# Kernel optimization log

Measured on AMD Instinct MI355X. Metric: run time of the kernel, lower is better.

The kernel has to match this reference:

```python
import jax, jax.numpy as jnp
import numpy as np

N_PROT = 100_000; E_PROT = 1_600_000
N_LIG = 5_000;    E_LIG = 80_000
B_PROT = 64; B_LIG = 1
SEQ = 130; D = 45; K = 4; DIN = 74
PROT_DIMS = [DIN, 50, 45, 45]
LIG_DIMS  = [DIN, 50, 45, 45, 45]
HEAD = [SEQ * D, 2000, 1000, 500, 1]


def setup_inputs() -> dict:
    key = jax.random.key(0)
    ks = iter(jax.random.split(key, 64))
    def rn(shape, scale=1.0):
        return jax.random.normal(next(ks), shape, jnp.float32) * scale
    inp = {
        "prot_x": rn((N_PROT, DIN)),
        "lig_x": rn((N_LIG, DIN)),
    }
    for pref, dims in (("prot", PROT_DIMS), ("lig", LIG_DIMS)):
        for i in range(len(dims) - 1):
            fan_in = (K + 1) * dims[i]
            inp[f"{pref}_W{i}"] = rn((fan_in, dims[i + 1]), fan_in ** -0.5)
            inp[f"{pref}_b{i}"] = jnp.zeros((dims[i + 1],), jnp.float32)
    inp["qkv_w"] = rn((D, 3 * D), D ** -0.5)
    inp["qkv_b"] = jnp.zeros((3 * D,), jnp.float32)
    inp["proj_w"] = rn((D, D), D ** -0.5)
    inp["proj_b"] = jnp.zeros((D,), jnp.float32)
    for i in range(3):
        inp[f"h{i}_w"] = rn((HEAD[i], HEAD[i + 1]), HEAD[i] ** -0.5)
        inp[f"h{i}_b"] = jnp.zeros((HEAD[i + 1],), jnp.float32)
    inp["fc_w"] = rn((HEAD[3], HEAD[4]), HEAD[3] ** -0.5)
    inp["fc_b"] = jnp.zeros((HEAD[4],), jnp.float32)
    inp["prot_src"] = jax.random.randint(next(ks), (E_PROT,), 0, N_PROT, jnp.int32)
    inp["prot_dst"] = jax.random.randint(next(ks), (E_PROT,), 0, N_PROT, jnp.int32)
    # deterministic contiguous subgraph ids guarantee all 64 pockets are non-empty
    inp["prot_gid"] = (jnp.arange(N_PROT) * B_PROT // N_PROT).astype(jnp.int32)
    inp["lig_src"] = jax.random.randint(next(ks), (E_LIG,), 0, N_LIG, jnp.int32)
    inp["lig_dst"] = jax.random.randint(next(ks), (E_LIG,), 0, N_LIG, jnp.int32)
    inp["lig_gid"] = jnp.zeros((N_LIG,), jnp.int32)
    inp["training"] = 0
    return inp


def _tagconv(x, src, dst, W, b, n):
    # DGL TAGConv: h_{k+1} = D^{-1/2} A D^{-1/2} h_k ; out = [h_0..h_K] @ W + b
    deg = jax.ops.segment_sum(jnp.ones_like(dst, x.dtype), dst, num_segments=n)
    norm = jnp.where(deg > 0, deg, 1.0) ** -0.5  # clamp(min=1)^-0.5
    hops = [x]
    h = x
    for _ in range(K):
        h = norm[:, None] * jax.ops.segment_sum((h * norm[:, None])[src], dst, num_segments=n)
        hops.append(h)
    return jnp.concatenate(hops, axis=-1) @ W + b


def _l2norm(x):
    # F.normalize(dim=1): x / max(||x||_2, eps)
    return x / jnp.maximum(jnp.linalg.norm(x, axis=1, keepdims=True), 1e-12)


def _gnn(x, src, dst, gid, Ws, bs, n, ngraphs):
    for W, b in zip(Ws, bs):
        x = _l2norm(jax.nn.relu(_tagconv(x, src, dst, W, b, n)))
        # dropout is identity in eval mode
    return jax.ops.segment_max(x, gid, num_segments=ngraphs)  # DGL MaxPooling


def reference(prot_x, lig_x,
              prot_W0, prot_b0, prot_W1, prot_b1, prot_W2, prot_b2,
              lig_W0, lig_b0, lig_W1, lig_b1, lig_W2, lig_b2, lig_W3, lig_b3,
              qkv_w, qkv_b, proj_w, proj_b,
              h0_w, h0_b, h1_w, h1_b, h2_w, h2_b, fc_w, fc_b,
              prot_src, prot_dst, prot_gid, lig_src, lig_dst, lig_gid, training):
    prot_rep = _gnn(prot_x, prot_src, prot_dst, prot_gid,
                    [prot_W0, prot_W1, prot_W2], [prot_b0, prot_b1, prot_b2],
                    N_PROT, B_PROT)                    # [B_PROT, 45]
    lig_rep = _gnn(lig_x, lig_src, lig_dst, lig_gid,
                   [lig_W0, lig_W1, lig_W2, lig_W3], [lig_b0, lig_b1, lig_b2, lig_b3],
                   N_LIG, B_LIG)                       # [B_LIG, 45]
    n_seq = B_LIG + B_PROT
    seq = jnp.concatenate([lig_rep, prot_rep], axis=0)  # [n_seq, 45]
    seq = jnp.pad(seq, ((0, SEQ - n_seq), (0, 0)))[None]  # [1, 130, 45]

    # eye-based mask exactly as the torch code builds it
    idx = jnp.arange(SEQ)
    valid = idx < n_seq
    mask = jnp.eye(SEQ, dtype=jnp.float32) * (valid[:, None] & valid[None, :])
    mask = mask.at[:, n_seq - 1].set(1.0)
    mask = mask.at[n_seq - 1, :].set(1.0)
    mask = mask.at[n_seq - 1, n_seq - 1].set(0.0)

    qkv = seq @ qkv_w + qkv_b                 # [1, 130, 135]
    q, k, v = jnp.split(qkv, 3, axis=-1)      # single head, head_dim = 45
    attn = jnp.einsum("bqd,bkd->bqk", q, k) * (D ** -0.5)
    attn = jnp.where(mask[None] == 0, -1e9, attn)
    attn = jax.nn.softmax(attn, axis=-1)
    out = jnp.einsum("bqk,bkd->bqd", attn, v) @ proj_w + proj_b  # [1,130,45]

    out = out.reshape(1, SEQ * D)             # [1, 5850]
    for w, b in ((h0_w, h0_b), (h1_w, h1_b), (h2_w, h2_b)):
        out = jax.nn.relu(out @ w + b)        # head dropout off in eval
    return jax.nn.sigmoid(out @ fc_w + fc_b)  # [1, 1]
```

## Files before the change

kernel.cpp:

```cpp
#include <hip/hip_runtime.h>
#include <hip/hip_fp16.h>
#include <cstddef>
#include <cstdint>

namespace {

constexpr int NPROT = 100000;
constexpr int EPROT = 1600000;
constexpr int NLIG  = 5000;
constexpr int ELIG  = 80000;


__global__ void hist_kernel(const int* __restrict__ dst, int* __restrict__ cnt, int e) {
  int i = blockIdx.x * 256 + threadIdx.x;
  if (i < e) atomicAdd(&cnt[dst[i]], 1);
}

__global__ void scan1_kernel(const int* __restrict__ cnt, int* __restrict__ rp,
                             int* __restrict__ bsum, float* __restrict__ nrm, int n) {
  __shared__ int wsum[4];
  int t = threadIdx.x;
  int base = blockIdx.x * 1024 + t * 4;
  int v0 = 0, v1 = 0, v2 = 0, v3 = 0;
  if (base + 3 < n) {
    int4 val = *(const int4*)(cnt + base);
    v0 = val.x; v1 = val.y; v2 = val.z; v3 = val.w;
  } else if (base < n) {
    v0 = cnt[base];
    if (base + 1 < n) v1 = cnt[base + 1];
    if (base + 2 < n) v2 = cnt[base + 2];
  }
  if (base < n)     nrm[base]     = 1.0f / sqrtf(fmaxf((float)v0, 1.0f));
  if (base + 1 < n) nrm[base + 1] = 1.0f / sqrtf(fmaxf((float)v1, 1.0f));
  if (base + 2 < n) nrm[base + 2] = 1.0f / sqrtf(fmaxf((float)v2, 1.0f));
  if (base + 3 < n) nrm[base + 3] = 1.0f / sqrtf(fmaxf((float)v3, 1.0f));
  int ts = v0 + v1 + v2 + v3;
  int lane = t & 63, wv = t >> 6;
  int incl = ts;
  #pragma unroll
  for (int off = 1; off < 64; off <<= 1) {
    int o = __shfl_up(incl, off, 64);
    if (lane >= off) incl += o;
  }
  if (lane == 63) wsum[wv] = incl;
  __syncthreads();
  int woff = 0;
  #pragma unroll
  for (int i = 0; i < 4; ++i) if (i < wv) woff += wsum[i];
  int excl = woff + incl - ts;
  int o0 = excl, o1 = o0 + v0, o2 = o1 + v1, o3 = o2 + v2;
  if (base + 3 < n) {
    *(int4*)(rp + base) = make_int4(o0, o1, o2, o3);
  } else if (base < n) {
    rp[base] = o0;
    if (base + 1 < n) rp[base + 1] = o1;
    if (base + 2 < n) rp[base + 2] = o2;
  }
  if (t == 255) bsum[blockIdx.x] = woff + incl;
}

__global__ void scan2_kernel(int* __restrict__ bsum, int nb, int* __restrict__ rp_end) {
  __shared__ int s[256];
  int t = threadIdx.x;
  int v = (t < nb) ? bsum[t] : 0;
  s[t] = v;
  __syncthreads();
  int val = v;
  for (int off = 1; off < 256; off <<= 1) {
    int add = (t >= off) ? s[t - off] : 0;
    __syncthreads();
    val += add;
    s[t] = val;
    __syncthreads();
  }
  if (t < nb) bsum[t] = val - v;
  if (t == 255) *rp_end = val;
}

__global__ void scan3_kernel(int* __restrict__ rp, const int* __restrict__ bsum, int n) {
  int i = blockIdx.x * 256 + threadIdx.x;
  if (i < n) rp[i] += bsum[i >> 10];
}

__global__ void scatter_kernel(const int* __restrict__ src, const int* __restrict__ dst,
                               const int* __restrict__ rp, int* __restrict__ cur,
                               int* __restrict__ col, int e) {
  int i = blockIdx.x * 256 + threadIdx.x;
  if (i < e) {
    int d = dst[i];
    int p = rp[d] + atomicAdd(&cur[d], 1);
    col[p] = src[i];
  }
}


__device__ __forceinline__ float2 cvt_h2(uint32_t u) {
  __half2 h = *reinterpret_cast<__half2*>(&u);
  return make_float2(__low2float(h), __high2float(h));
}

__global__ void gather_all_kernel(const __half* __restrict__ gin, const int* __restrict__ rp,
                                  const int* __restrict__ col, const float* __restrict__ nrm,
                                  __half* __restrict__ gout, int n, int nbn) {
  int pass = blockIdx.x / nbn;
  int bid = blockIdx.x - pass * nbn;
  int lane = threadIdx.x & 63, wv = threadIdx.x >> 6;
  int q = lane >> 4, r = lane & 15;
  int e_slot = r >> 2, f4 = r & 3;
  int v = bid * 16 + wv * 4 + q;
  bool vok = (v < n);
  int beg = 0, deg = 0;
  if (vok) { beg = rp[v]; deg = rp[v + 1] - beg; }
  const __half* gc = gin + (size_t)pass * n * 16;
  __half* go = gout + (size_t)pass * n * 16;
  float a0 = 0.f, a1 = 0.f, a2 = 0.f, a3 = 0.f;
  for (int base = 0; __any(base < deg); base += 16) {
    int ec = (base + r < deg) ? col[beg + base + r] : -1;
    #pragma unroll
    for (int js = 0; js < 16; js += 4) {
      int sl = (q << 4) + js + e_slot;
      int s0 = __shfl(ec, sl, 64);
      int idx = (s0 >= 0) ? s0 : 0;
      float m = (s0 >= 0) ? 1.f : 0.f;
      uint2 u = *(const uint2*)(gc + (size_t)idx * 16 + (f4 << 2));
      float2 p0 = cvt_h2(u.x), p1 = cvt_h2(u.y);
      a0 += m * p0.x; a1 += m * p0.y; a2 += m * p1.x; a3 += m * p1.y;
    }
  }
  a0 += __shfl_xor(a0, 4, 64);  a1 += __shfl_xor(a1, 4, 64);
  a2 += __shfl_xor(a2, 4, 64);  a3 += __shfl_xor(a3, 4, 64);
  a0 += __shfl_xor(a0, 8, 64);  a1 += __shfl_xor(a1, 8, 64);
  a2 += __shfl_xor(a2, 8, 64);  a3 += __shfl_xor(a3, 8, 64);
  if (vok && e_slot == 0) {
    float nm = nrm[v];
    float nm2 = nm * nm;
    __half2 w0 = __floats2half2_rn(a0 * nm2, a1 * nm2);
    __half2 w1 = __floats2half2_rn(a2 * nm2, a3 * nm2);
    uint2 st;
    st.x = *reinterpret_cast<uint32_t*>(&w0);
    st.y = *reinterpret_cast<uint32_t*>(&w1);
    *(uint2*)(go + ((size_t)v << 4) + (f4 << 2)) = st;
  }
}

template<int DIN>
__global__ void init_g0_kernel(const float* __restrict__ x, const float* __restrict__ nrm,
                               __half* __restrict__ g0, int n) {
  constexpr int PD = (DIN + 15) & ~15;
  int lane = threadIdx.x & 63;
  int v = blockIdx.x * 4 + (threadIdx.x >> 6);
  if (v >= n) return;
  float nm = nrm[v];
  for (int f = lane; f < PD; f += 64) {
    float val = (f < DIN) ? x[(size_t)v * DIN + f] * nm : 0.f;
    g0[(((size_t)(f >> 4) * n + v) << 4) + (f & 15)] = __float2half(val);
  }
}

__global__ void padw_kernel(const float* __restrict__ W, float* __restrict__ Wp,
                            int din, int dout, int pd) {
  int i = blockIdx.x * 256 + threadIdx.x;
  int total = 5 * pd * dout;
  if (i >= total) return;
  int f = i / dout, j = i - f * dout;
  int hop = f / pd, rem = f - hop * pd;
  Wp[i] = (rem < din) ? W[(size_t)(hop * din + rem) * dout + j] : 0.f;
}

template<int DIN, int DOUT, bool LAST>
__global__ __launch_bounds__(256) void combine_kernel(
    const __half* __restrict__ gbase, const float* __restrict__ nrm,
    const float* __restrict__ Wp, const float* __restrict__ bias,
    __half* __restrict__ gnext, float* __restrict__ Xout, int n) {
  constexpr int PD  = (DIN + 15) & ~15;
  constexpr int NCH = PD / 16;
  constexpr int PDN = (DOUT + 15) & ~15;
  constexpr int QO  = ((DOUT + 7) / 8) * 2;
  __shared__ float ssq[4 * 64];
  int lane = threadIdx.x & 63, wv = threadIdx.x >> 6;
  int v = blockIdx.x * 64 + lane;
  bool vok = (v < n);
  int vc = vok ? v : 0;
  const size_t slabh = (size_t)n * 80;
  int cofs = __builtin_amdgcn_readfirstlane(wv) * QO;
  float acc[QO];
  #pragma unroll
  for (int jj = 0; jj < QO; ++jj) acc[jj] = 0.f;
  const float* wb = Wp + cofs;
  for (int hop = 0; hop < 5; ++hop) {
    const __half* hrow = gbase + (size_t)hop * slabh + ((size_t)vc << 4);
    #pragma unroll 1
    for (int ch = 0; ch < NCH; ++ch) {
      uint4 u0 = *(const uint4*)hrow;
      uint4 u1 = *(const uint4*)(hrow + 8);
      float h[16];
      {
        float2 p;
        p = cvt_h2(u0.x); h[0] = p.x; h[1] = p.y;
        p = cvt_h2(u0.y); h[2] = p.x; h[3] = p.y;
        p = cvt_h2(u0.z); h[4] = p.x; h[5] = p.y;
        p = cvt_h2(u0.w); h[6] = p.x; h[7] = p.y;
        p = cvt_h2(u1.x); h[8] = p.x; h[9] = p.y;
        p = cvt_h2(u1.y); h[10] = p.x; h[11] = p.y;
        p = cvt_h2(u1.z); h[12] = p.x; h[13] = p.y;
        p = cvt_h2(u1.w); h[14] = p.x; h[15] = p.y;
      }
      #pragma unroll
      for (int s = 0; s < 16; ++s) {
        #pragma unroll
        for (int jj = 0; jj < QO; ++jj) acc[jj] += h[s] * wb[s * DOUT + jj];
      }
      wb += 16 * DOUT;
      hrow += ((size_t)n << 4);
    }
  }
  float rn = 1.f / nrm[vc];
  float ss = 0.f;
  #pragma unroll
  for (int jj = 0; jj < QO; ++jj) {
    int j = cofs + jj;
    float y = (j < DOUT) ? fmaxf(bias[j] + acc[jj] * rn, 0.f) : 0.f;
    acc[jj] = y;
    ss += y * y;
  }
  ssq[wv * 64 + lane] = ss;
  __syncthreads();
  if (!vok) return;
  float tot = ssq[lane] + ssq[64 + lane] + ssq[128 + lane] + ssq[192 + lane];
  float sc = 1.f / fmaxf(sqrtf(tot), 1e-12f);
  if (LAST) {
    #pragma unroll
    for (int jj = 0; jj < QO; ++jj) {
      int j = cofs + jj;
      if (j < DOUT) Xout[(size_t)v * DOUT + j] = acc[jj] * sc;
    }
  } else {
    float nm = nrm[v];
    #pragma unroll
    for (int jj = 0; jj < QO; jj += 2) {
      int j0 = cofs + jj;
      float a = (j0 < DOUT) ? acc[jj] * sc * nm : 0.f;
      float b = (j0 + 1 < DOUT) ? acc[jj + 1] * sc * nm : 0.f;
      int ch = j0 >> 4, s = j0 & 15;
      *(__half2*)(gnext + (((size_t)ch * n + v) << 4) + s) = __floats2half2_rn(a, b);
    }
    if (wv == 3) {
      #pragma unroll
      for (int j0 = 4 * QO; j0 < PDN; j0 += 2) {
        int ch = j0 >> 4, s = j0 & 15;
        *(__half2*)(gnext + (((size_t)ch * n + v) << 4) + s) = __floats2half2_rn(0.f, 0.f);
      }
    }
  }
}


template<int DIN, int GS, int DOUT>
__global__ void init_gemm_kernel(const float* __restrict__ x, const float* __restrict__ nrm,
                                 const float* __restrict__ W, const float* __restrict__ bias,
                                 __half* __restrict__ gout, float* __restrict__ y, int n) {
  int lane = threadIdx.x & 63;
  int v = blockIdx.x * 4 + (threadIdx.x >> 6);
  if (v >= n) return;
  float nm = nrm[v];
  const float* xr = x + (size_t)v * DIN;
  float hA = (lane < DIN) ? xr[lane] : 0.f;
  float hB = 0.f;
  if constexpr (DIN > 64) { if (lane + 64 < DIN) hB = xr[lane + 64]; }
  __half* go = gout + (size_t)v * GS;
  if (lane < DIN) go[lane] = __float2half(hA * nm);
  if constexpr (DIN > 64) { if (lane + 64 < DIN) go[lane + 64] = __float2half(hB * nm); }
  int cl = (lane < DOUT) ? lane : 0;
  float acc = bias[cl];
  const float* Wk = W + cl;
  #pragma unroll
  for (int f = 0; f < DIN; ++f) {
    float hf = (f < 64) ? __shfl(hA, f, 64) : __shfl(hB, f - 64, 64);
    acc += hf * Wk[(size_t)f * DOUT];
  }
  if (lane < DOUT) y[(size_t)v * DOUT + lane] = acc;
}

template<int DIN, int GS, int DOUT, bool WRITEG, bool FINAL>
__global__ void fused_hop_kernel(const __half* __restrict__ gin, const int* __restrict__ rp,
                                 const int* __restrict__ col, const float* __restrict__ nrm,
                                 const float* __restrict__ W, __half* __restrict__ gout,
                                 float* __restrict__ y, float* __restrict__ Xout,
                                 int k, int n) {
  int lane = threadIdx.x & 63;
  int v = blockIdx.x * 4 + (threadIdx.x >> 6);
  if (v >= n) return;
  int beg = rp[v], end = rp[v + 1];
  float a0 = 0.f, a1 = 0.f;
  for (int base = beg; base < end; base += 64) {
    int m = end - base; if (m > 64) m = 64;
    int myc = (lane < m) ? col[base + lane] : 0;
    int j = 0;
    for (; j + 8 <= m; j += 8) {
      int ss[8];
      float t0[8], t1[8];
      #pragma unroll
      for (int u = 0; u < 8; ++u) ss[u] = __shfl(myc, j + u, 64);
      #pragma unroll
      for (int u = 0; u < 8; ++u) {
        const __half* rr = gin + (size_t)ss[u] * GS;
        t0[u] = (lane < DIN) ? __half2float(rr[lane]) : 0.f;
        if constexpr (DIN > 64) t1[u] = (lane + 64 < DIN) ? __half2float(rr[lane + 64]) : 0.f;
      }
      #pragma unroll
      for (int u = 0; u < 8; ++u) {
        a0 += t0[u];
        if constexpr (DIN > 64) a1 += t1[u];
      }
    }
    for (; j < m; ++j) {
      int s = __shfl(myc, j, 64);
      const __half* rr = gin + (size_t)s * GS;
      if (lane < DIN) a0 += __half2float(rr[lane]);
      if constexpr (DIN > 64) { if (lane + 64 < DIN) a1 += __half2float(rr[lane + 64]); }
    }
  }
  float nm = nrm[v];
  float hA = a0 * nm, hB = a1 * nm;
  if (WRITEG) {
    __half* go = gout + (size_t)v * GS;
    if (lane < DIN) go[lane] = __float2half(hA * nm);
    if constexpr (DIN > 64) { if (lane + 64 < DIN) go[lane + 64] = __float2half(hB * nm); }
  }
  int cl = (lane < DOUT) ? lane : 0;
  float acc = 0.f;
  if (lane < DOUT) acc = y[(size_t)v * DOUT + lane];
  const float* Wk = W + (size_t)k * DIN * DOUT + cl;
  #pragma unroll
  for (int f = 0; f < DIN; ++f) {
    float hf = (f < 64) ? __shfl(hA, f, 64) : __shfl(hB, f - 64, 64);
    acc += hf * Wk[(size_t)f * DOUT];
  }
  if constexpr (FINAL) {
    float val = (lane < DOUT) ? fmaxf(acc, 0.f) : 0.f;
    float ss2 = val * val;
    #pragma unroll
    for (int off2 = 32; off2 > 0; off2 >>= 1) ss2 += __shfl_xor(ss2, off2, 64);
    float scale = 1.f / fmaxf(sqrtf(ss2), 1e-12f);
    if (lane < DOUT) Xout[(size_t)v * DOUT + lane] = val * scale;
  } else {
    if (lane < DOUT) y[(size_t)v * DOUT + lane] = acc;
  }
}

__global__ void segmax_kernel(const float* __restrict__ X, const int* __restrict__ gid,
                              float* __restrict__ rep, int n, int row_off) {
  __shared__ float tab[4][45];
  __shared__ int gids[256];
  int t = threadIdx.x;
  for (int i = t; i < 4 * 45; i += 256) ((float*)tab)[i] = 0.f;
  int v0 = blockIdx.x * 256;
  int vend = v0 + 256; if (vend > n) vend = n;
  int nv = vend - v0;
  if (t < nv) gids[t] = gid[v0 + t];
  __syncthreads();
  int g0 = gids[0];
  int total = nv * 45;
  for (int i = t; i < total; i += 256) {
    int vl = i / 45, j = i - vl * 45;
    float val = X[(size_t)(v0 + vl) * 45 + j];
    int rel = gids[vl] - g0;
    if (rel >= 0 && rel < 4)
      atomicMax((unsigned int*)&tab[rel][j], __float_as_uint(val));
    else
      atomicMax((unsigned int*)&rep[(size_t)(row_off + gids[vl]) * 45 + j], __float_as_uint(val));
  }
  __syncthreads();
  for (int i = t; i < 4 * 45; i += 256) {
    float val = ((float*)tab)[i];
    if (val > 0.f) {
      int rel = i / 45, j = i - rel * 45;
      atomicMax((unsigned int*)&rep[(size_t)(row_off + g0 + rel) * 45 + j], __float_as_uint(val));
    }
  }
}


__global__ void qkv_kernel(const float* __restrict__ rep, const float* __restrict__ w,
                           const float* __restrict__ b, float* __restrict__ qkv) {
  int i = blockIdx.x;
  int t = threadIdx.x;
  __shared__ float sr[45];
  if (t < 45) sr[t] = (i < 65) ? rep[(size_t)i * 45 + t] : 0.f;
  __syncthreads();
  if (t < 135) {
    float acc = b[t];
    #pragma unroll 5
    for (int d = 0; d < 45; ++d) acc += sr[d] * w[d * 135 + t];
    qkv[(size_t)i * 135 + t] = acc;
  }
}

__global__ void attn_kernel(const float* __restrict__ qkv, const float* __restrict__ proj_w,
                            const float* __restrict__ proj_b, float* __restrict__ ctx) {
  int i = blockIdx.x;
  int t = threadIdx.x;
  __shared__ float q[45];
  __shared__ float p[130];
  __shared__ float red[256];
  __shared__ float ao[45];
  if (t < 45) q[t] = qkv[(size_t)i * 135 + t];
  __syncthreads();
  float s = -1e30f;
  if (t < 130) {
    int j = t;
    float dot = 0.f;
    #pragma unroll 5
    for (int d = 0; d < 45; ++d) dot += q[d] * qkv[(size_t)j * 135 + 45 + d];
    dot *= 0.14907119849998599f;
    bool mz;
    if (i == 64 && j == 64) mz = true;
    else if (i == 64 || j == 64) mz = false;
    else mz = !(i == j && i < 65);
    s = mz ? -1e9f : dot;
  }
  red[t] = s;
  __syncthreads();
  #pragma unroll
  for (int off = 128; off > 0; off >>= 1) {
    if (t < off) red[t] = fmaxf(red[t], red[t + off]);
    __syncthreads();
  }
  float mx = red[0];
  __syncthreads();
  float e = (t < 130) ? expf(s - mx) : 0.f;
  red[t] = e;
  __syncthreads();
  #pragma unroll
  for (int off = 128; off > 0; off >>= 1) {
    if (t < off) red[t] += red[t + off];
    __syncthreads();
  }
  float denom = red[0];
  __syncthreads();
  if (t < 130) p[t] = e / denom;
  __syncthreads();
  if (t < 45) {
    float acc = 0.f;
    for (int j = 0; j < 130; ++j) acc += p[j] * qkv[(size_t)j * 135 + 90 + t];
    ao[t] = acc;
  }
  __syncthreads();
  if (t < 45) {
    float pr = proj_b[t];
    #pragma unroll 5
    for (int e2 = 0; e2 < 45; ++e2) pr += ao[e2] * proj_w[e2 * 45 + t];
    ctx[(size_t)i * 45 + t] = pr;
  }
}


__global__ void bias_init_kernel(const float* __restrict__ b, float* __restrict__ out, int n) {
  int i = blockIdx.x * 256 + threadIdx.x;
  if (i < n) out[i] = b[i];
}

template<bool RELU_IN>
__global__ void fc_splitk_kernel(const float* __restrict__ x, const float* __restrict__ W,
                                 float* __restrict__ out, int nin, int nout, int kchunk) {
  __shared__ float xs[1024];
  int k0 = blockIdx.y * kchunk;
  int k1 = k0 + kchunk; if (k1 > nin) k1 = nin;
  int len = k1 - k0;
  for (int i = threadIdx.x; i < len; i += blockDim.x) {
    float v = x[k0 + i];
    xs[i] = RELU_IN ? fmaxf(v, 0.f) : v;
  }
  __syncthreads();
  int j = blockIdx.x * blockDim.x + threadIdx.x;
  if (j < nout) {
    float acc = 0.f;
    const float* Wp = W + (size_t)k0 * nout + j;
    for (int i = 0; i < len; ++i) acc += xs[i] * Wp[(size_t)i * nout];
    atomicAdd(&out[j], acc);
  }
}

__global__ void final_fc_kernel(const float* __restrict__ x, const float* __restrict__ W,
                                const float* __restrict__ b, float* __restrict__ out) {
  __shared__ float red[512];
  int t = threadIdx.x;
  float acc = 0.f;
  if (t < 500) acc = fmaxf(x[t], 0.f) * W[t];
  red[t] = acc;
  __syncthreads();
  #pragma unroll
  for (int off = 256; off > 0; off >>= 1) {
    if (t < off) red[t] += red[t + off];
    __syncthreads();
  }
  if (t == 0) {
    float z = red[0] + b[0];
    out[0] = 1.f / (1.f + expf(-z));
  }
}


struct Bufs {
  __half* slabs;
  __half *ligA, *ligB;
  float *X, *Y, *nrm, *Wp;
  int *cnt, *cur, *rp, *col, *bsum;
};

template<int DIN, int DOUT, bool LAST>
void run_layer_prot(const Bufs& g, const float* W, const float* b, int n, hipStream_t st) {
  constexpr int PD = (DIN + 15) & ~15;
  constexpr int NPASS = PD / 16;
  int nbn = (n + 15) / 16;
  size_t slabh = (size_t)n * 80;
  for (int k = 1; k <= 4; ++k)
    gather_all_kernel<<<NPASS * nbn, 256, 0, st>>>(g.slabs + (size_t)(k - 1) * slabh,
                                                   g.rp, g.col, g.nrm,
                                                   g.slabs + (size_t)k * slabh, n, nbn);
  int wtotal = 5 * PD * DOUT;
  padw_kernel<<<(wtotal + 255) / 256, 256, 0, st>>>(W, g.Wp, DIN, DOUT, PD);
  combine_kernel<DIN, DOUT, LAST><<<(n + 63) / 64, 256, 0, st>>>(
      g.slabs, g.nrm, g.Wp, b, g.slabs, g.X, n);
}

template<int DIN, int GS, int DOUT>
void run_layer_lig(const float* xin, const Bufs& g, const float* W, const float* b,
                   int n, hipStream_t st) {
  int nb = (n + 3) / 4;
  init_gemm_kernel<DIN, GS, DOUT><<<nb, 256, 0, st>>>(xin, g.nrm, W, b, g.ligA, g.Y, n);
  const __half* gin = g.ligA;
  __half* gout = g.ligB;
  for (int k = 1; k <= 4; ++k) {
    if (k < 4)
      fused_hop_kernel<DIN, GS, DOUT, true, false><<<nb, 256, 0, st>>>(gin, g.rp, g.col, g.nrm, W, gout, g.Y, g.X, k, n);
    else
      fused_hop_kernel<DIN, GS, DOUT, false, true><<<nb, 256, 0, st>>>(gin, g.rp, g.col, g.nrm, W, gout, g.Y, g.X, 4, n);
    __half* t = (__half*)gin; gin = gout; gout = t;
  }
}

void build_csr(const int* src, const int* dst, const Bufs& g, int n, int e, hipStream_t st) {
  hipMemsetAsync(g.cnt, 0, (size_t)n * 4, st);
  hipMemsetAsync(g.cur, 0, (size_t)n * 4, st);
  hist_kernel<<<(e + 255) / 256, 256, 0, st>>>(dst, g.cnt, e);
  int nb1 = (n + 1023) / 1024;
  scan1_kernel<<<nb1, 256, 0, st>>>(g.cnt, g.rp, g.bsum, g.nrm, n);
  scan2_kernel<<<1, 256, 0, st>>>(g.bsum, nb1, g.rp + n);
  scan3_kernel<<<(n + 255) / 256, 256, 0, st>>>(g.rp, g.bsum, n);
  scatter_kernel<<<(e + 255) / 256, 256, 0, st>>>(src, dst, g.rp, g.cur, g.col, e);
}

}

extern "C" void kernel_launch(void* const* d_in, const int* in_sizes, int n_in,
                              void* d_out, int out_size, void* d_ws, size_t ws_size,
                              hipStream_t stream) {
  (void)in_sizes; (void)n_in; (void)out_size;

  const float* prot_x = (const float*)d_in[0];
  const float* lig_x  = (const float*)d_in[1];
  const float* pW[3] = {(const float*)d_in[2], (const float*)d_in[4], (const float*)d_in[6]};
  const float* pB[3] = {(const float*)d_in[3], (const float*)d_in[5], (const float*)d_in[7]};
  const float* lW[4] = {(const float*)d_in[8], (const float*)d_in[10], (const float*)d_in[12], (const float*)d_in[14]};
  const float* lB[4] = {(const float*)d_in[9], (const float*)d_in[11], (const float*)d_in[13], (const float*)d_in[15]};
  const float* qkv_w = (const float*)d_in[16];
  const float* qkv_b = (const float*)d_in[17];
  const float* proj_w = (const float*)d_in[18];
  const float* proj_b = (const float*)d_in[19];
  const float* h0_w = (const float*)d_in[20];
  const float* h0_b = (const float*)d_in[21];
  const float* h1_w = (const float*)d_in[22];
  const float* h1_b = (const float*)d_in[23];
  const float* h2_w = (const float*)d_in[24];
  const float* h2_b = (const float*)d_in[25];
  const float* fc_w = (const float*)d_in[26];
  const float* fc_b = (const float*)d_in[27];
  const int* prot_src = (const int*)d_in[28];
  const int* prot_dst = (const int*)d_in[29];
  const int* prot_gid = (const int*)d_in[30];
  const int* lig_src  = (const int*)d_in[31];
  const int* lig_dst  = (const int*)d_in[32];
  const int* lig_gid  = (const int*)d_in[33];

  char* w = (char*)d_ws;
  size_t off = 0;
  auto alloc = [&](size_t bytes) -> void* {
    void* p = w + off;
    off += (bytes + 255) & ~(size_t)255;
    return p;
  };
  __half* slabs = (__half*)alloc((size_t)5 * NPROT * 80 * 2);
  __half* ligA  = (__half*)alloc((size_t)NLIG * 96 * 2);
  __half* ligB  = (__half*)alloc((size_t)NLIG * 96 * 2);
  float* X   = (float*)alloc((size_t)NPROT * 45 * 4);
  float* Y   = (float*)alloc((size_t)NLIG * 50 * 4);
  float* nrm = (float*)alloc((size_t)NPROT * 4);
  float* Wp  = (float*)alloc((size_t)5 * 80 * 50 * 4 + 256);
  int* cnt   = (int*)alloc((size_t)NPROT * 4);
  int* cur   = (int*)alloc((size_t)NPROT * 4);
  int* rp    = (int*)alloc(((size_t)NPROT + 1) * 4);
  int* colb  = (int*)alloc((size_t)EPROT * 4);
  int* bsum  = (int*)alloc((size_t)256 * 4);
  float* rep = (float*)alloc((size_t)65 * 45 * 4);
  float* qkvb = (float*)alloc((size_t)130 * 135 * 4);
  float* ctx  = (float*)alloc((size_t)5850 * 4);
  float* hb0  = (float*)alloc((size_t)2000 * 4);
  float* hb1  = (float*)alloc((size_t)1000 * 4);
  float* hb2  = (float*)alloc((size_t)500 * 4);
  if (off > ws_size) return;

  hipMemsetAsync(rep, 0, (size_t)65 * 45 * 4, stream);

  Bufs g{slabs, ligA, ligB, X, Y, nrm, Wp, cnt, cur, rp, colb, bsum};

  build_csr(prot_src, prot_dst, g, NPROT, EPROT, stream);
  init_g0_kernel<74><<<(NPROT + 3) / 4, 256, 0, stream>>>(prot_x, g.nrm, g.slabs, NPROT);
  run_layer_prot<74, 50, false>(g, pW[0], pB[0], NPROT, stream);
  run_layer_prot<50, 45, false>(g, pW[1], pB[1], NPROT, stream);
  run_layer_prot<45, 45, true >(g, pW[2], pB[2], NPROT, stream);
  segmax_kernel<<<(NPROT + 255) / 256, 256, 0, stream>>>(g.X, prot_gid, rep, NPROT, 1);

  build_csr(lig_src, lig_dst, g, NLIG, ELIG, stream);
  run_layer_lig<74, 96, 50>(lig_x, g, lW[0], lB[0], NLIG, stream);
  run_layer_lig<50, 64, 45>(g.X, g, lW[1], lB[1], NLIG, stream);
  run_layer_lig<45, 64, 45>(g.X, g, lW[2], lB[2], NLIG, stream);
  run_layer_lig<45, 64, 45>(g.X, g, lW[3], lB[3], NLIG, stream);
  segmax_kernel<<<(NLIG + 255) / 256, 256, 0, stream>>>(g.X, lig_gid, rep, NLIG, 0);

  qkv_kernel<<<130, 256, 0, stream>>>(rep, qkv_w, qkv_b, qkvb);
  attn_kernel<<<130, 256, 0, stream>>>(qkvb, proj_w, proj_b, ctx);

  bias_init_kernel<<<8, 256, 0, stream>>>(h0_b, hb0, 2000);
  fc_splitk_kernel<false><<<dim3(8, 8), 256, 0, stream>>>(ctx, h0_w, hb0, 5850, 2000, 732);
  bias_init_kernel<<<4, 256, 0, stream>>>(h1_b, hb1, 1000);
  fc_splitk_kernel<true><<<dim3(4, 4), 256, 0, stream>>>(hb0, h1_w, hb1, 2000, 1000, 500);
  bias_init_kernel<<<2, 256, 0, stream>>>(h2_b, hb2, 500);
  fc_splitk_kernel<true><<<dim3(2, 2), 256, 0, stream>>>(hb1, h2_w, hb2, 1000, 500, 500);
  final_fc_kernel<<<1, 512, 0, stream>>>(hb2, fc_w, fc_b, (float*)d_out);
}
```

Before: 1.422 ms.

## Degree-sort vertices for gather and bucket edges before CSR scatter

Builds a permutation of vertices sorted by in-degree using a counting sort, and the gather kernel now processes vertices in that order so 4-vertex groups within a wavefront have similar degree and less divergence. Edge scatter becomes two passes: edges are first binned by destination range into a temporary buffer reusing the slab memory, then scattered into CSR, so the col writes are more local. The gather inner loop also exits early once all lanes pass their degree and uses fmaf. This adds several small kernels and an extra pass over the edges, and the vertex permutation makes gather output writes scattered.

```diff
diff --git a/kernel.cpp b/kernel.cpp
--- a/kernel.cpp
+++ b/kernel.cpp
@@ -82,14 +82,80 @@
   if (i < n) rp[i] += bsum[i >> 10];
 }
 
-__global__ void scatter_kernel(const int* __restrict__ src, const int* __restrict__ dst,
-                               const int* __restrict__ rp, int* __restrict__ cur,
-                               int* __restrict__ col, int e) {
+
+__global__ void dhist_kernel(const int* __restrict__ cnt, int* __restrict__ dh, int n) {
+  int i = blockIdx.x * 256 + threadIdx.x;
+  if (i < n) atomicAdd(&dh[min(cnt[i], 255)], 1);
+}
+
+__global__ void dscan_kernel(const int* __restrict__ dh, int* __restrict__ dcur) {
+  __shared__ int s[256];
+  int t = threadIdx.x;
+  int v = dh[t];
+  s[t] = v;
+  __syncthreads();
+  int val = v;
+  for (int off = 1; off < 256; off <<= 1) {
+    int add = (t >= off) ? s[t - off] : 0;
+    __syncthreads();
+    val += add;
+    s[t] = val;
+    __syncthreads();
+  }
+  dcur[t] = val - v;
+}
+
+__global__ void dscat_kernel(const int* __restrict__ cnt, int* __restrict__ dcur,
+                             int* __restrict__ vorder, int n) {
+  int i = blockIdx.x * 256 + threadIdx.x;
+  if (i < n) {
+    int b = min(cnt[i], 255);
+    int p = atomicAdd(&dcur[b], 1);
+    vorder[p] = i;
+  }
+}
+
+
+__global__ void gcur_init_kernel(const int* __restrict__ rp, int* __restrict__ gcur, int n) {
+  int t = threadIdx.x;
+  if (t < 64) gcur[t] = rp[min(t << 11, n)];
+}
+
+__global__ void scat1_kernel(const int* __restrict__ src, const int* __restrict__ dst,
+                             int* __restrict__ gcur, uint2* __restrict__ ebuf, int e) {
+  __shared__ int lh[64], lb[64];
+  int t = threadIdx.x;
+  if (t < 64) lh[t] = 0;
+  __syncthreads();
+  int base = blockIdx.x * 4096;
+  int d[16], rk[16];
+  #pragma unroll
+  for (int j = 0; j < 16; ++j) {
+    int i = base + j * 256 + t;
+    if (i < e) {
+      d[j] = dst[i];
+      rk[j] = atomicAdd(&lh[min(d[j] >> 11, 63)], 1);
+    }
+  }
+  __syncthreads();
+  if (t < 64 && lh[t] > 0) lb[t] = atomicAdd(&gcur[t], lh[t]);
+  __syncthreads();
+  #pragma unroll
+  for (int j = 0; j < 16; ++j) {
+    int i = base + j * 256 + t;
+    if (i < e)
+      ebuf[lb[min(d[j] >> 11, 63)] + rk[j]] = make_uint2((unsigned)src[i], (unsigned)d[j]);
+  }
+}
+
+__global__ void scat2_kernel(const uint2* __restrict__ ebuf, const int* __restrict__ rp,
+                             int* __restrict__ cur, int* __restrict__ col, int e) {
   int i = blockIdx.x * 256 + threadIdx.x;
   if (i < e) {
-    int d = dst[i];
-    int p = rp[d] + atomicAdd(&cur[d], 1);
-    col[p] = src[i];
+    uint2 p = ebuf[i];
+    int d = (int)p.y;
+    int q = rp[d] + atomicAdd(&cur[d], 1);
+    col[q] = (int)p.x;
   }
 }
 
@@ -101,14 +167,16 @@
 
 __global__ void gather_all_kernel(const __half* __restrict__ gin, const int* __restrict__ rp,
                                   const int* __restrict__ col, const float* __restrict__ nrm,
+                                  const int* __restrict__ vorder,
                                   __half* __restrict__ gout, int n, int nbn) {
   int pass = blockIdx.x / nbn;
   int bid = blockIdx.x - pass * nbn;
   int lane = threadIdx.x & 63, wv = threadIdx.x >> 6;
   int q = lane >> 4, r = lane & 15;
   int e_slot = r >> 2, f4 = r & 3;
-  int v = bid * 16 + wv * 4 + q;
-  bool vok = (v < n);
+  int vi = bid * 16 + wv * 4 + q;
+  bool vok = (vi < n);
+  int v = vok ? vorder[vi] : 0;
   int beg = 0, deg = 0;
   if (vok) { beg = rp[v]; deg = rp[v + 1] - beg; }
   const __half* gc = gin + (size_t)pass * n * 16;
@@ -118,13 +186,15 @@
     int ec = (base + r < deg) ? col[beg + base + r] : -1;
     #pragma unroll
     for (int js = 0; js < 16; js += 4) {
+      if (js > 0 && __all(base + js >= deg)) break;
       int sl = (q << 4) + js + e_slot;
       int s0 = __shfl(ec, sl, 64);
       int idx = (s0 >= 0) ? s0 : 0;
       float m = (s0 >= 0) ? 1.f : 0.f;
       uint2 u = *(const uint2*)(gc + (size_t)idx * 16 + (f4 << 2));
       float2 p0 = cvt_h2(u.x), p1 = cvt_h2(u.y);
-      a0 += m * p0.x; a1 += m * p0.y; a2 += m * p1.x; a3 += m * p1.y;
+      a0 = fmaf(m, p0.x, a0); a1 = fmaf(m, p0.y, a1);
+      a2 = fmaf(m, p1.x, a2); a3 = fmaf(m, p1.y, a3);
     }
   }
   a0 += __shfl_xor(a0, 4, 64);  a1 += __shfl_xor(a1, 4, 64);
@@ -505,7 +575,8 @@
   __half* slabs;
   __half *ligA, *ligB;
   float *X, *Y, *nrm, *Wp;
-  int *cnt, *cur, *rp, *col, *bsum;
+  int *cnt, *cur, *rp, *col, *bsum, *vorder, *dh, *dcur, *gcur;
+  uint2* ebuf;
 };
 
 template<int DIN, int DOUT, bool LAST>
@@ -516,7 +587,7 @@
   size_t slabh = (size_t)n * 80;
   for (int k = 1; k <= 4; ++k)
     gather_all_kernel<<<NPASS * nbn, 256, 0, st>>>(g.slabs + (size_t)(k - 1) * slabh,
-                                                   g.rp, g.col, g.nrm,
+                                                   g.rp, g.col, g.nrm, g.vorder,
                                                    g.slabs + (size_t)k * slabh, n, nbn);
   int wtotal = 5 * PD * DOUT;
   padw_kernel<<<(wtotal + 255) / 256, 256, 0, st>>>(W, g.Wp, DIN, DOUT, PD);
@@ -543,12 +614,18 @@
 void build_csr(const int* src, const int* dst, const Bufs& g, int n, int e, hipStream_t st) {
   hipMemsetAsync(g.cnt, 0, (size_t)n * 4, st);
   hipMemsetAsync(g.cur, 0, (size_t)n * 4, st);
+  hipMemsetAsync(g.dh, 0, 256 * 4, st);
   hist_kernel<<<(e + 255) / 256, 256, 0, st>>>(dst, g.cnt, e);
   int nb1 = (n + 1023) / 1024;
   scan1_kernel<<<nb1, 256, 0, st>>>(g.cnt, g.rp, g.bsum, g.nrm, n);
   scan2_kernel<<<1, 256, 0, st>>>(g.bsum, nb1, g.rp + n);
   scan3_kernel<<<(n + 255) / 256, 256, 0, st>>>(g.rp, g.bsum, n);
-  scatter_kernel<<<(e + 255) / 256, 256, 0, st>>>(src, dst, g.rp, g.cur, g.col, e);
+  dhist_kernel<<<(n + 255) / 256, 256, 0, st>>>(g.cnt, g.dh, n);
+  dscan_kernel<<<1, 256, 0, st>>>(g.dh, g.dcur);
+  dscat_kernel<<<(n + 255) / 256, 256, 0, st>>>(g.cnt, g.dcur, g.vorder, n);
+  gcur_init_kernel<<<1, 64, 0, st>>>(g.rp, g.gcur, n);
+  scat1_kernel<<<(e + 4095) / 4096, 256, 0, st>>>(src, dst, g.gcur, g.ebuf, e);
+  scat2_kernel<<<(e + 255) / 256, 256, 0, st>>>(g.ebuf, g.rp, g.cur, g.col, e);
 }
 
 }
@@ -602,6 +679,10 @@
   int* rp    = (int*)alloc(((size_t)NPROT + 1) * 4);
   int* colb  = (int*)alloc((size_t)EPROT * 4);
   int* bsum  = (int*)alloc((size_t)256 * 4);
+  int* vorder = (int*)alloc((size_t)NPROT * 4);
+  int* dh    = (int*)alloc((size_t)256 * 4);
+  int* dcur  = (int*)alloc((size_t)256 * 4);
+  int* gcur  = (int*)alloc((size_t)64 * 4);
   float* rep = (float*)alloc((size_t)65 * 45 * 4);
   float* qkvb = (float*)alloc((size_t)130 * 135 * 4);
   float* ctx  = (float*)alloc((size_t)5850 * 4);
@@ -612,7 +693,8 @@
 
   hipMemsetAsync(rep, 0, (size_t)65 * 45 * 4, stream);
 
-  Bufs g{slabs, ligA, ligB, X, Y, nrm, Wp, cnt, cur, rp, colb, bsum};
+  Bufs g{slabs, ligA, ligB, X, Y, nrm, Wp, cnt, cur, rp, colb, bsum,
+         vorder, dh, dcur, gcur, (uint2*)slabs };
 
   build_csr(prot_src, prot_dst, g, NPROT, EPROT, stream);
   init_g0_kernel<74><<<(NPROT + 3) / 4, 256, 0, stream>>>(prot_x, g.nrm, g.slabs, NPROT);
```

Measured after the change: 2.136 ms. 50.2% more time.
